# Kernel optimization log

Hardware: AMD Instinct MI355X
Metric: run time of the kernel (lower is better)

The kernel has to match this reference:

```python
import jax, jax.numpy as jnp
import numpy as np

MARGIN = 1.0   # TripletLoss(margin) init arg
EPS = 1e-6     # torch F.pairwise_distance eps used by nn.TripletMarginLoss
INF = 1e9

N, D_EMB, N_CLASSES = 8192, 1024, 128


def setup_inputs() -> dict:
    key = jax.random.key(0)
    k1, k2 = jax.random.split(key)
    embeddings = jax.random.normal(k1, (N, D_EMB), dtype=jnp.float32)
    target = jax.random.randint(k2, (N,), 0, N_CLASSES, dtype=jnp.int64 if jax.config.jax_enable_x64 else jnp.int32)
    return {"embeddings": embeddings, "target": target}


def _mine_and_loss(embeddings, target):
    # Vectorized, deterministic equivalent of the per-anchor random mining loop:
    # full pairwise L2 distance matrix via a GEMM (compute-bound core).
    sq = jnp.sum(embeddings * embeddings, axis=1)                      # [N]
    d2 = sq[:, None] + sq[None, :] - 2.0 * (embeddings @ embeddings.T)  # [N, N]
    Dm = jnp.sqrt(jnp.maximum(d2, 0.0))                                 # [N, N]

    same = target[:, None] == target[None, :]
    eye = jnp.eye(target.shape[0], dtype=bool)
    pos_mask = same & ~eye          # valid positives (same class, not self)
    neg_mask = ~same                # valid negatives (different class)

    # Positive: hardest (farthest) same-class sample (deterministic stand-in
    # for the original's random positive draw).
    pos_scores = jnp.where(pos_mask, Dm, -INF)
    pos_idx = jnp.argmax(pos_scores, axis=1)                           # [N]
    d_p = jnp.max(pos_scores, axis=1)                                  # [N]

    # Negative: semi-hard (d_p < d_n < d_p + margin), pick the closest such
    # negative; if none exists, fall back to the overall hardest (min-dist)
    # negative -- mirrors the loop's early-break vs. min_dist fallback.
    semi = neg_mask & (Dm > d_p[:, None]) & (Dm < (d_p + MARGIN)[:, None])
    has_semi = jnp.any(semi, axis=1)
    neg_semi = jnp.argmin(jnp.where(semi, Dm, INF), axis=1)
    neg_hard = jnp.argmin(jnp.where(neg_mask, Dm, INF), axis=1)
    neg_idx = jnp.where(has_semi, neg_semi, neg_hard)                  # [N]

    # nn.TripletMarginLoss(margin, p=2): mean(relu(d(a,p) - d(a,n) + margin))
    # with torch's pairwise_distance eps added to the difference.
    a = embeddings
    p = embeddings[pos_idx]
    n = embeddings[neg_idx]
    dp = jnp.sqrt(jnp.sum((a - p + EPS) ** 2, axis=1))
    dn = jnp.sqrt(jnp.sum((a - n + EPS) ** 2, axis=1))
    return jnp.mean(jax.nn.relu(dp - dn + MARGIN))


def reference(embeddings, target):
    return _mine_and_loss(embeddings, target)
```

## Files before the change

kernel.cpp:

```cpp
#include <hip/hip_runtime.h>
#include <hip/hip_bf16.h>

#define N 8192
#define D 1024
#define MARGIN 1.0f
#define EPS 1e-6f

typedef __attribute__((ext_vector_type(8))) short bf16x8;
typedef __attribute__((ext_vector_type(4))) float f32x4;
typedef __attribute__((ext_vector_type(8))) _Float16 f16x8;
typedef __attribute__((ext_vector_type(4))) _Float16 f16x4;
typedef __attribute__((ext_vector_type(8))) unsigned short u16x8;

__device__ inline unsigned short f2bf(float x) {
    unsigned u = __float_as_uint(x);
    unsigned r = (u + 0x7FFFu + ((u >> 16) & 1u)) >> 16;
    return (unsigned short)r;
}

__device__ inline float h2f(unsigned hb) {
    return (float)__builtin_bit_cast(_Float16, (unsigned short)hb);
}

__global__ __launch_bounds__(256) void prep_kernel(const float* __restrict__ E,
                                                   unsigned short* __restrict__ Ebf,
                                                   float* __restrict__ sq) {
    const int r = blockIdx.x;
    const int tid = threadIdx.x;
    const float4 v = ((const float4*)(E + (size_t)r * D))[tid];
    ushort4 o;
    o.x = f2bf(v.x); o.y = f2bf(v.y); o.z = f2bf(v.z); o.w = f2bf(v.w);
    ((ushort4*)(Ebf + (size_t)r * D))[tid] = o;
    float s = v.x * v.x + v.y * v.y + v.z * v.z + v.w * v.w;
    for (int off = 32; off > 0; off >>= 1) s += __shfl_down(s, off);
    __shared__ float red[4];
    const int lane = tid & 63, wave = tid >> 6;
    if (lane == 0) red[wave] = s;
    __syncthreads();
    if (tid == 0) sq[r] = red[0] + red[1] + red[2] + red[3];
}

__global__ __launch_bounds__(256) void cls_kernel(const int* __restrict__ target,
                                                  unsigned char* __restrict__ cls) {
    const int t = blockIdx.x * 256 + threadIdx.x;
    cls[t] = (unsigned char)target[t];
}

__global__ __launch_bounds__(256) void gemm_kernel(const unsigned short* __restrict__ E,
                                                   const float* __restrict__ sq,
                                                   _Float16* __restrict__ D2h) {
    __shared__ char smem[128 * 136 * 2];
    unsigned short* As = (unsigned short*)smem;
    unsigned short* Bs = (unsigned short*)(smem + 8192);
    _Float16* Ts = (_Float16*)smem;

    const int tid = threadIdx.x;
    const int lane = tid & 63;
    const int wave = tid >> 6;
    const int wm = wave & 1, wn = wave >> 1;

    const int l = blockIdx.x;
    int by = (int)((sqrtf(8.0f * (float)l + 1.0f) - 1.0f) * 0.5f);
    while ((by + 1) * (by + 2) / 2 <= l) ++by;
    while (by * (by + 1) / 2 > l) --by;
    const int bx = l - by * (by + 1) / 2;
    const int rm = by * 128;
    const int cn = bx * 128;

    const int srow = tid >> 2;
    const int scol = (tid & 3) * 8;

    const unsigned short* gA = E + (size_t)(rm + srow) * D + scol;
    const unsigned short* gB = E + (size_t)(cn + srow) * D + scol;

    f32x4 acc[4][4] = {};

    const int kq = (lane >> 4) * 8;
    const int mr = lane & 15;

    for (int k0 = 0; k0 < D; k0 += 32) {
        __builtin_amdgcn_global_load_lds(
            (const __attribute__((address_space(1))) unsigned int*)(gA + k0),
            (__attribute__((address_space(3))) unsigned int*)((char*)As + wave * 1024), 16, 0, 0);
        __builtin_amdgcn_global_load_lds(
            (const __attribute__((address_space(1))) unsigned int*)(gA + (size_t)64 * D + k0),
            (__attribute__((address_space(3))) unsigned int*)((char*)As + 4096 + wave * 1024), 16, 0, 0);
        __builtin_amdgcn_global_load_lds(
            (const __attribute__((address_space(1))) unsigned int*)(gB + k0),
            (__attribute__((address_space(3))) unsigned int*)((char*)Bs + wave * 1024), 16, 0, 0);
        __builtin_amdgcn_global_load_lds(
            (const __attribute__((address_space(1))) unsigned int*)(gB + (size_t)64 * D + k0),
            (__attribute__((address_space(3))) unsigned int*)((char*)Bs + 4096 + wave * 1024), 16, 0, 0);
        __syncthreads();

        bf16x8 af[4], bfr[4];
#pragma unroll
        for (int mi = 0; mi < 4; ++mi)
            af[mi] = *(const bf16x8*)(As + (wm * 64 + mi * 16 + mr) * 32 + kq);
#pragma unroll
        for (int ni = 0; ni < 4; ++ni)
            bfr[ni] = *(const bf16x8*)(Bs + (wn * 64 + ni * 16 + mr) * 32 + kq);
#pragma unroll
        for (int mi = 0; mi < 4; ++mi)
#pragma unroll
            for (int ni = 0; ni < 4; ++ni)
                acc[mi][ni] = __builtin_amdgcn_mfma_f32_16x16x32_bf16(af[mi], bfr[ni], acc[mi][ni], 0, 0, 0);
        __syncthreads();
    }

    const int crow = (lane >> 4) * 4;
    const int ccol = lane & 15;
    const bool offdiag = (bx != by);
    float sqj[4];
#pragma unroll
    for (int ni = 0; ni < 4; ++ni)
        sqj[ni] = sq[cn + wn * 64 + ni * 16 + ccol];
#pragma unroll
    for (int mi = 0; mi < 4; ++mi) {
        const int lrow = wm * 64 + mi * 16 + crow;
        const int i0 = rm + lrow;
        float sqi[4];
#pragma unroll
        for (int r = 0; r < 4; ++r) sqi[r] = sq[i0 + r];
#pragma unroll
        for (int ni = 0; ni < 4; ++ni) {
            const int lcol = wn * 64 + ni * 16 + ccol;
            const int j = cn + lcol;
            f16x4 tv;
#pragma unroll
            for (int r = 0; r < 4; ++r) {
                float d2 = fmaxf(sqi[r] + sqj[ni] - 2.0f * acc[mi][ni][r], 0.0f);
                _Float16 h = (_Float16)d2;
                D2h[(size_t)(i0 + r) * N + j] = h;
                tv[r] = h;
            }
            if (offdiag)
                *(f16x4*)(Ts + (size_t)lcol * 136 + lrow) = tv;
        }
    }
    if (offdiag) {
        __syncthreads();
#pragma unroll
        for (int it = 0; it < 8; ++it) {
            const int rt = it * 16 + (tid >> 4);
            const int seg = tid & 15;
            f16x8 v = *(const f16x8*)(Ts + (size_t)rt * 136 + seg * 8);
            *(f16x8*)(D2h + (size_t)(cn + rt) * N + rm + seg * 8) = v;
        }
    }
}

__global__ __launch_bounds__(256) void mine_kernel(const _Float16* __restrict__ D2h,
                                                   const unsigned char* __restrict__ cls,
                                                   float* __restrict__ loss_arr) {
    const int i = blockIdx.x;
    const int tid = threadIdx.x;
    const int lane = tid & 63, wave = tid >> 6;
    const unsigned tcb = cls[i];
    const unsigned short* row = (const unsigned short*)(D2h + (size_t)i * N);

    u16x8 v[4];
    unsigned long long c8[4];
#pragma unroll
    for (int it = 0; it < 4; ++it) {
        v[it] = *(const u16x8*)(row + it * 2048 + tid * 8);
        c8[it] = *(const unsigned long long*)(cls + it * 2048 + tid * 8);
    }

    unsigned pm = 0u, nm = 0xFFFFu;
#pragma unroll
    for (int it = 0; it < 4; ++it) {
#pragma unroll
        for (int e = 0; e < 8; ++e) {
            const unsigned hb = v[it][e];
            const bool s = ((unsigned)(c8[it] >> (8 * e)) & 0xFFu) == tcb;
            pm = max(pm, s ? hb : 0u);
            nm = min(nm, s ? 0xFFFFu : hb);
        }
    }
    for (int off = 1; off < 64; off <<= 1) {
        pm = max(pm, (unsigned)__shfl_xor((int)pm, off));
        nm = min(nm, (unsigned)__shfl_xor((int)nm, off));
    }
    __shared__ unsigned redp[4], redn[4], reds[4];
    if (lane == 0) { redp[wave] = pm; redn[wave] = nm; }
    __syncthreads();
    pm = max(max(redp[0], redp[1]), max(redp[2], redp[3]));
    nm = min(min(redn[0], redn[1]), min(redn[2], redn[3]));
    const unsigned lob = pm;

    unsigned sm = 0xFFFFu;
#pragma unroll
    for (int it = 0; it < 4; ++it) {
#pragma unroll
        for (int e = 0; e < 8; ++e) {
            const unsigned hb = v[it][e];
            sm = min(sm, hb > lob ? hb : 0xFFFFu);
        }
    }
    for (int off = 1; off < 64; off <<= 1)
        sm = min(sm, (unsigned)__shfl_xor((int)sm, off));
    if (lane == 0) reds[wave] = sm;
    __syncthreads();
    if (tid == 0) {
        sm = min(min(reds[0], reds[1]), min(reds[2], reds[3]));
        const float lo = h2f(lob);
        const float dp = sqrtf(lo);
        const float hw = dp + MARGIN;
        const float hi = hw * hw;
        const float smv = h2f(sm);
        const float dn2 = (smv < hi) ? smv : h2f(nm);
        loss_arr[i] = fmaxf(dp - sqrtf(dn2) + MARGIN, 0.0f);
    }
}

__global__ __launch_bounds__(256) void reduce_kernel(const float* __restrict__ loss_arr,
                                                     float* __restrict__ out) {
    const int tid = threadIdx.x;
    float s = 0.0f;
    for (int k = tid; k < N; k += 256) s += loss_arr[k];
    for (int off = 32; off > 0; off >>= 1) s += __shfl_down(s, off);
    __shared__ float red[4];
    const int lane = tid & 63, wave = tid >> 6;
    if (lane == 0) red[wave] = s;
    __syncthreads();
    if (tid == 0) out[0] = (red[0] + red[1] + red[2] + red[3]) * (1.0f / N);
}

extern "C" void kernel_launch(void* const* d_in, const int* in_sizes, int n_in,
                              void* d_out, int out_size, void* d_ws, size_t ws_size,
                              hipStream_t stream) {
    const float* E = (const float*)d_in[0];
    const int* target = (const int*)d_in[1];
    float* out = (float*)d_out;
    char* ws = (char*)d_ws;

    unsigned short* Ebf = (unsigned short*)ws;
    float* sq        = (float*)(ws + (size_t)16777216);
    float* loss_arr  = (float*)(ws + (size_t)16809984);
    unsigned char* cls = (unsigned char*)(ws + (size_t)16842752);
    _Float16* D2h    = (_Float16*)(ws + (size_t)16875520);

    prep_kernel<<<N, 256, 0, stream>>>(E, Ebf, sq);
    cls_kernel<<<N / 256, 256, 0, stream>>>(target, cls);
    gemm_kernel<<<2080, 256, 0, stream>>>(Ebf, sq, D2h);
    mine_kernel<<<N, 256, 0, stream>>>(D2h, cls, loss_arr);
    reduce_kernel<<<1, 256, 0, stream>>>(loss_arr, out);
}
```

Measured before the change: 208.1 us.

## Rewrite symmetric GEMM as 256x256-tile, 8-wave, LDS-pipelined kernel

The distance GEMM moves from 128x128 tiles with 4 waves to 256x256 tiles with 8 waves. It uses a double-buffered 128KB dynamic LDS ring with XOR-swizzled layout, issues next-stage global_load_lds during MFMA phases, and uses setprio and vmcnt waits in place of full syncthreads. The transposed mirror write now goes directly to global as strided f16x4 stores, dropping the LDS transpose. The aim is to overlap loads with compute, cut bank conflicts and raise operand reuse, at the cost of fewer blocks (528), heavy LDS use that allows only one block per CU, and uncoalesced transposed stores.

```diff
diff --git a/kernel.cpp b/kernel.cpp
--- a/kernel.cpp
+++ b/kernel.cpp
@@ -46,106 +46,118 @@
     cls[t] = (unsigned char)target[t];
 }
 
-__global__ __launch_bounds__(256) void gemm_kernel(const unsigned short* __restrict__ E,
-                                                   const float* __restrict__ sq,
-                                                   _Float16* __restrict__ D2h) {
-    __shared__ char smem[128 * 136 * 2];
-    unsigned short* As = (unsigned short*)smem;
-    unsigned short* Bs = (unsigned short*)(smem + 8192);
-    _Float16* Ts = (_Float16*)smem;
+
+#define SLOT_0A0 0
+#define SLOT_0A1 16384
+#define SLOT_0B0 32768
+#define SLOT_0B1 49152
+#define SLOT_1A0 65536
+#define SLOT_1A1 81920
+#define SLOT_1B0 98304
+#define SLOT_1B1 114688
+
+#define STAGE(slotOff, baseRow, kcol) do {                                              \
+    const unsigned short* _s0 = E + (size_t)((baseRow) + (tid >> 2)) * D + (kcol) + stc * 8; \
+    __builtin_amdgcn_global_load_lds(                                                    \
+        (const __attribute__((address_space(1))) unsigned int*)_s0,                      \
+        (__attribute__((address_space(3))) unsigned int*)(smem + (slotOff) + wave * 1024), 16, 0, 0); \
+    const unsigned short* _s1 = _s0 + (size_t)128 * D;                                   \
+    __builtin_amdgcn_global_load_lds(                                                    \
+        (const __attribute__((address_space(1))) unsigned int*)_s1,                      \
+        (__attribute__((address_space(3))) unsigned int*)(smem + (slotOff) + 8192 + wave * 1024), 16, 0, 0); \
+} while (0)
+
+#define PHASE(b, ks, mq, LOADB, SLOT_ST, TILE_ST, BASE_ST, KH_ST, DO_VM) do {            \
+    const char* _As = smem + (b) * 65536 + (ks) * 16384;                                 \
+    const char* _Bs = smem + (b) * 65536 + 32768 + (ks) * 16384;                         \
+    if (LOADB) {                                                                         \
+        _Pragma("unroll") for (int nj = 0; nj < 4; ++nj)                                 \
+            bfr[nj] = *(const bf16x8*)(_Bs + (wn * 64 + nj * 16 + mr) * 64 + swz);       \
+    }                                                                                    \
+    bf16x8 af[4];                                                                        \
+    _Pragma("unroll") for (int mi = 0; mi < 4; ++mi)                                     \
+        af[mi] = *(const bf16x8*)(_As + (wm * 128 + (mq) * 64 + mi * 16 + mr) * 64 + swz); \
+    STAGE(SLOT_ST, BASE_ST, (TILE_ST) * 64 + (KH_ST));                                   \
+    __asm__ __volatile__("s_barrier" ::: "memory");                                      \
+    __builtin_amdgcn_s_setprio(1);                                                       \
+    _Pragma("unroll") for (int mi = 0; mi < 4; ++mi)                                     \
+        _Pragma("unroll") for (int nj = 0; nj < 4; ++nj)                                 \
+            acc[(mq) * 4 + mi][nj] = __builtin_amdgcn_mfma_f32_16x16x32_bf16(            \
+                af[mi], bfr[nj], acc[(mq) * 4 + mi][nj], 0, 0, 0);                       \
+    __builtin_amdgcn_s_setprio(0);                                                       \
+    if (DO_VM) __asm__ __volatile__("s_waitcnt vmcnt(6)" ::: "memory");                  \
+    __asm__ __volatile__("s_barrier" ::: "memory");                                      \
+} while (0)
+
+__global__ __launch_bounds__(512, 2) void gemm_kernel(const unsigned short* __restrict__ E,
+                                                      const float* __restrict__ sq,
+                                                      _Float16* __restrict__ D2h) {
+    extern __shared__ char smem[];
 
     const int tid = threadIdx.x;
     const int lane = tid & 63;
     const int wave = tid >> 6;
-    const int wm = wave & 1, wn = wave >> 1;
+    const int wm = wave >> 2;
+    const int wn = wave & 3;
+    const int mr = lane & 15;
+    const int q = lane >> 4;
+    const int swz = ((q ^ ((mr >> 1) & 3)) << 4);
+    const int stc = (tid & 3) ^ ((tid >> 3) & 3);
 
     const int l = blockIdx.x;
     int by = (int)((sqrtf(8.0f * (float)l + 1.0f) - 1.0f) * 0.5f);
     while ((by + 1) * (by + 2) / 2 <= l) ++by;
     while (by * (by + 1) / 2 > l) --by;
     const int bx = l - by * (by + 1) / 2;
-    const int rm = by * 128;
-    const int cn = bx * 128;
-
-    const int srow = tid >> 2;
-    const int scol = (tid & 3) * 8;
-
-    const unsigned short* gA = E + (size_t)(rm + srow) * D + scol;
-    const unsigned short* gB = E + (size_t)(cn + srow) * D + scol;
-
-    f32x4 acc[4][4] = {};
-
-    const int kq = (lane >> 4) * 8;
-    const int mr = lane & 15;
-
-    for (int k0 = 0; k0 < D; k0 += 32) {
-        __builtin_amdgcn_global_load_lds(
-            (const __attribute__((address_space(1))) unsigned int*)(gA + k0),
-            (__attribute__((address_space(3))) unsigned int*)((char*)As + wave * 1024), 16, 0, 0);
-        __builtin_amdgcn_global_load_lds(
-            (const __attribute__((address_space(1))) unsigned int*)(gA + (size_t)64 * D + k0),
-            (__attribute__((address_space(3))) unsigned int*)((char*)As + 4096 + wave * 1024), 16, 0, 0);
-        __builtin_amdgcn_global_load_lds(
-            (const __attribute__((address_space(1))) unsigned int*)(gB + k0),
-            (__attribute__((address_space(3))) unsigned int*)((char*)Bs + wave * 1024), 16, 0, 0);
-        __builtin_amdgcn_global_load_lds(
-            (const __attribute__((address_space(1))) unsigned int*)(gB + (size_t)64 * D + k0),
-            (__attribute__((address_space(3))) unsigned int*)((char*)Bs + 4096 + wave * 1024), 16, 0, 0);
-        __syncthreads();
-
-        bf16x8 af[4], bfr[4];
-#pragma unroll
-        for (int mi = 0; mi < 4; ++mi)
-            af[mi] = *(const bf16x8*)(As + (wm * 64 + mi * 16 + mr) * 32 + kq);
-#pragma unroll
-        for (int ni = 0; ni < 4; ++ni)
-            bfr[ni] = *(const bf16x8*)(Bs + (wn * 64 + ni * 16 + mr) * 32 + kq);
-#pragma unroll
-        for (int mi = 0; mi < 4; ++mi)
-#pragma unroll
-            for (int ni = 0; ni < 4; ++ni)
-                acc[mi][ni] = __builtin_amdgcn_mfma_f32_16x16x32_bf16(af[mi], bfr[ni], acc[mi][ni], 0, 0, 0);
-        __syncthreads();
-    }
-
-    const int crow = (lane >> 4) * 4;
-    const int ccol = lane & 15;
-    const bool offdiag = (bx != by);
+    const int rm = by * 256;
+    const int cn = bx * 256;
+
+    f32x4 acc[8][4] = {};
+    bf16x8 bfr[4];
+
+    STAGE(SLOT_0A0, rm, 0);
+    STAGE(SLOT_0B0, cn, 0);
+    STAGE(SLOT_0A1, rm, 32);
+    STAGE(SLOT_0B1, cn, 32);
+    STAGE(SLOT_1A0, rm, 64);
+    __asm__ __volatile__("s_waitcnt vmcnt(6)" ::: "memory");
+    __asm__ __volatile__("s_barrier" ::: "memory");
+
+    for (int i = 0; i < 8; ++i) {
+        const int kt = 2 * i;
+        const int t2 = (kt + 2 < 16) ? kt + 2 : 15;
+        const int t3 = (kt + 3 < 16) ? kt + 3 : 15;
+        PHASE(0, 0, 0, 1, SLOT_1B0, kt + 1, cn, 0, 0);
+        PHASE(0, 0, 1, 0, SLOT_1A1, kt + 1, rm, 32, 1);
+        PHASE(0, 1, 0, 1, SLOT_1B1, kt + 1, cn, 32, 0);
+        PHASE(0, 1, 1, 0, SLOT_0A0, t2, rm, 0, 1);
+        PHASE(1, 0, 0, 1, SLOT_0B0, t2, cn, 0, 0);
+        PHASE(1, 0, 1, 0, SLOT_0A1, t2, rm, 32, 1);
+        PHASE(1, 1, 0, 1, SLOT_0B1, t2, cn, 32, 0);
+        PHASE(1, 1, 1, 0, SLOT_1A0, t3, rm, 0, 1);
+    }
+
+    const int crow = q * 4;
     float sqj[4];
 #pragma unroll
-    for (int ni = 0; ni < 4; ++ni)
-        sqj[ni] = sq[cn + wn * 64 + ni * 16 + ccol];
-#pragma unroll
-    for (int mi = 0; mi < 4; ++mi) {
-        const int lrow = wm * 64 + mi * 16 + crow;
-        const int i0 = rm + lrow;
-        float sqi[4];
-#pragma unroll
-        for (int r = 0; r < 4; ++r) sqi[r] = sq[i0 + r];
-#pragma unroll
-        for (int ni = 0; ni < 4; ++ni) {
-            const int lcol = wn * 64 + ni * 16 + ccol;
-            const int j = cn + lcol;
+    for (int nj = 0; nj < 4; ++nj) sqj[nj] = sq[cn + wn * 64 + nj * 16 + mr];
+    const bool offd = (bx != by);
+#pragma unroll
+    for (int mg = 0; mg < 8; ++mg) {
+        const int i0 = rm + wm * 128 + mg * 16 + crow;
+        const f32x4 sqi = *(const f32x4*)(sq + i0);
+#pragma unroll
+        for (int nj = 0; nj < 4; ++nj) {
+            const int j = cn + wn * 64 + nj * 16 + mr;
             f16x4 tv;
 #pragma unroll
             for (int r = 0; r < 4; ++r) {
-                float d2 = fmaxf(sqi[r] + sqj[ni] - 2.0f * acc[mi][ni][r], 0.0f);
-                _Float16 h = (_Float16)d2;
+                const float d2 = fmaxf(sqi[r] + sqj[nj] - 2.0f * acc[mg][nj][r], 0.0f);
+                const _Float16 h = (_Float16)d2;
+                tv[r] = h;
                 D2h[(size_t)(i0 + r) * N + j] = h;
-                tv[r] = h;
             }
-            if (offdiag)
-                *(f16x4*)(Ts + (size_t)lcol * 136 + lrow) = tv;
-        }
-    }
-    if (offdiag) {
-        __syncthreads();
-#pragma unroll
-        for (int it = 0; it < 8; ++it) {
-            const int rt = it * 16 + (tid >> 4);
-            const int seg = tid & 15;
-            f16x8 v = *(const f16x8*)(Ts + (size_t)rt * 136 + seg * 8);
-            *(f16x8*)(D2h + (size_t)(cn + rt) * N + rm + seg * 8) = v;
+            if (offd) *(f16x4*)(D2h + (size_t)j * N + i0) = tv;
         }
     }
 }
@@ -241,9 +253,16 @@
     unsigned char* cls = (unsigned char*)(ws + (size_t)16842752);
     _Float16* D2h    = (_Float16*)(ws + (size_t)16875520);
 
+    static bool attr_set = false;
+    if (!attr_set) {
+        hipFuncSetAttribute((const void*)gemm_kernel,
+                            hipFuncAttributeMaxDynamicSharedMemorySize, 131072);
+        attr_set = true;
+    }
+
     prep_kernel<<<N, 256, 0, stream>>>(E, Ebf, sq);
     cls_kernel<<<N / 256, 256, 0, stream>>>(target, cls);
-    gemm_kernel<<<2080, 256, 0, stream>>>(Ebf, sq, D2h);
+    gemm_kernel<<<528, 512, 131072, stream>>>(Ebf, sq, D2h);
     mine_kernel<<<N, 256, 0, stream>>>(D2h, cls, loss_arr);
     reduce_kernel<<<1, 256, 0, stream>>>(loss_arr, out);
 }
```

Measured after the change: 215.5 us. 3.6% more time.
